# Optimization experiments

Measured on AMD Instinct MI355X. Metric: run time of the kernel, lower is better.

The kernel has to match this reference:

```python
import jax, jax.numpy as jnp
import numpy as np

N, M, D, IN_DIM, RF_DIM, N_REL, L, NQ = 50000, 800000, 64, 768, 768, 500, 2, 2048


def _leaky(x):
    return jnp.where(x >= 0, x, 0.01 * x)  # nn.LeakyReLU default slope


def _ln(x, g, b):
    mu = jnp.mean(x, axis=-1, keepdims=True)
    var = jnp.mean(jnp.square(x - mu), axis=-1, keepdims=True)
    return (x - mu) / jnp.sqrt(var + 1e-5) * g + b


def setup_inputs() -> dict:
    key = jax.random.key(0)
    ks = jax.random.split(key, 24)
    ht = jax.random.randint(ks[0], (M, 2), 0, N)
    # ensure every node receives >= 1 message (avoids 0/0 NaN, as real batches do)
    ht = ht.at[:N, 0].set(jnp.arange(N))
    r_tensor = jax.random.randint(ks[1], (M,), 0, N_REL)
    entity_feat = jax.random.normal(ks[2], (N, IN_DIM), dtype=jnp.float32)
    queries = jnp.zeros((M,), jnp.int32).at[:NQ].set(1)
    s = 0.02
    rel_table = jax.random.normal(ks[3], (N_REL, RF_DIM), dtype=jnp.float32)  # frozen
    inp = {
        "ht": ht, "r_tensor": r_tensor, "entity_feat": entity_feat, "queries": queries,
        "rel_table": rel_table,
        "W_ent": s * jax.random.normal(ks[4], (IN_DIM, D)), "b_ent": jnp.zeros((D,)),
        "g_ent": jnp.ones((D,)), "be_ent": jnp.zeros((D,)),
        "W_edge_in": s * jax.random.normal(ks[5], (RF_DIM, D)), "b_edge_in": jnp.zeros((D,)),
        "g_edge": jnp.ones((D,)), "be_edge": jnp.zeros((D,)),
        "mp_Wf": s * jax.random.normal(ks[6], (L, 2 * D, D)), "mp_bf": jnp.zeros((L, D)),
        "mp_Wb": s * jax.random.normal(ks[7], (L, 2 * D, D)), "mp_bb": jnp.zeros((L, D)),
        "mp_g": jnp.ones((L, D)), "mp_be": jnp.zeros((L, D)),
        "eu_W": s * jax.random.normal(ks[8], (L, 3 * D, D)), "eu_b": jnp.zeros((L, D)),
        "eu_g": jnp.ones((L, D)), "eu_be": jnp.zeros((L, D)),
        "cls_W1": s * jax.random.normal(ks[9], (6 * D, D)), "cls_b1": jnp.zeros((D,)),
        "cls_W2": s * jax.random.normal(ks[10], (D, 1)), "cls_b2": jnp.zeros((1,)),
    }
    return inp


def _forward(ht, r_tensor, queries, rel_table, entity_feat,
             W_ent, b_ent, g_ent, be_ent, W_edge_in, b_edge_in, g_edge, be_edge,
             mp_Wf, mp_bf, mp_Wb, mp_bb, mp_g, mp_be,
             eu_W, eu_b, eu_g, eu_be, cls_W1, cls_b1, cls_W2, cls_b2):
    H0 = _ln(_leaky(entity_feat @ W_ent + b_ent), g_ent, be_ent)      # n x d
    r_embed = rel_table[r_tensor]                                     # m x rf
    E0 = _ln(_leaky(r_embed @ W_edge_in + b_edge_in), g_edge, be_edge)  # m x d
    H, E = H0, E0
    heads, tails = ht[:, 0], ht[:, 1]
    dst = jnp.concatenate([tails, heads])                             # 2m
    ones = jnp.ones((2 * M,), H.dtype)
    cnt = jax.ops.segment_sum(ones, dst, num_segments=N)              # per-node msg count
    for l in range(L):
        # message calculation (fwd uses head reps, back uses tail reps)
        mf = jnp.concatenate([H[heads], E], axis=1) @ mp_Wf[l] + mp_bf[l]
        mb = jnp.concatenate([H[tails], E], axis=1) @ mp_Wb[l] + mp_bb[l]
        msgs = jnp.concatenate([mf, mb], axis=0)                      # 2m x d
        agg = jax.ops.segment_sum(msgs, dst, num_segments=N) / cnt[:, None]
        H = _ln(_leaky(agg) + H, mp_g[l], mp_be[l])
        # edge update
        triple = jnp.concatenate([H[heads], E, H[tails]], axis=1)     # m x 3d
        E = _ln(_leaky(triple @ eu_W[l] + eu_b[l]) + E, eu_g[l], eu_be[l])
    # triple classification on query edges
    qi = jnp.nonzero(queries, size=NQ)[0]
    htq = ht[qi]
    feat = jnp.concatenate([E[qi], E0[qi], H[htq[:, 0]], H0[htq[:, 0]],
                            H[htq[:, 1]], H0[htq[:, 1]]], axis=1)     # NQ x 6d
    out = _leaky(feat @ cls_W1 + cls_b1) @ cls_W2 + cls_b2            # NQ x 1
    return out


def reference(ht, r_tensor, entity_feat, queries, rel_table,
              W_ent, b_ent, g_ent, be_ent, W_edge_in, b_edge_in, g_edge, be_edge,
              mp_Wf, mp_bf, mp_Wb, mp_bb, mp_g, mp_be,
              eu_W, eu_b, eu_g, eu_be, cls_W1, cls_b1, cls_W2, cls_b2):
    return _forward(ht, r_tensor, queries, rel_table, entity_feat,
                    W_ent, b_ent, g_ent, be_ent, W_edge_in, b_edge_in, g_edge, be_edge,
                    mp_Wf, mp_bf, mp_Wb, mp_bb, mp_g, mp_be,
                    eu_W, eu_b, eu_g, eu_be, cls_W1, cls_b1, cls_W2, cls_b2)
```

## Files before the change

kernel.cpp:

```cpp
#include <hip/hip_runtime.h>
#include <hip/hip_bf16.h>
#include <cstdint>

constexpr int IN_DIM = 768;
constexpr int FB_ENT = 0;
constexpr int FB_L0  = 96;
constexpr int FB_L1  = 128;
constexpr int NFRAG  = 160;

typedef __attribute__((ext_vector_type(8))) short bf16x8;
typedef __attribute__((ext_vector_type(4))) float f32x4;

static __device__ __forceinline__ float leaky_(float x){ return x >= 0.0f ? x : 0.01f * x; }

static __device__ __forceinline__ float wsum_(float v){
#pragma unroll
  for (int m = 1; m < 64; m <<= 1) v += __shfl_xor(v, m, 64);
  return v;
}

static __device__ __forceinline__ float wln_(float v, float g, float be){
  float mu  = wsum_(v) * 0.015625f;
  float c   = v - mu;
  float var = wsum_(c * c) * 0.015625f;
  return c * rsqrtf(var + 1e-5f) * g + be;
}

template<int CTRL>
static __device__ __forceinline__ float dpp_radd(float x){
  const int t = __builtin_amdgcn_update_dpp(0, __float_as_int(x), CTRL, 0xf, 0xf, true);
  return x + __int_as_float(t);
}
static __device__ __forceinline__ float rowsum16_(float x){
  x = dpp_radd<0x121>(x);
  x = dpp_radd<0x122>(x);
  x = dpp_radd<0x124>(x);
  x = dpp_radd<0x128>(x);
  return x;
}

static __device__ __forceinline__ unsigned short f2bf(float x){
  return __bfloat16_as_ushort(__float2bfloat16(x));
}
static __device__ __forceinline__ float bf2f(unsigned short u){
  return __bfloat162float(__ushort_as_bfloat16(u));
}
static __device__ __forceinline__ void split4(const float4 a, ushort4& hi, ushort4& lo){
  hi.x = f2bf(a.x); lo.x = f2bf(a.x - bf2f(hi.x));
  hi.y = f2bf(a.y); lo.y = f2bf(a.y - bf2f(hi.y));
  hi.z = f2bf(a.z); lo.z = f2bf(a.z - bf2f(hi.z));
  hi.w = f2bf(a.w); lo.w = f2bf(a.w - bf2f(hi.w));
}

static __device__ __forceinline__ f32x4 mfma3(bf16x8 ah, bf16x8 al, bf16x8 wh, bf16x8 wl, f32x4 acc){
  acc = __builtin_amdgcn_mfma_f32_16x16x32_bf16(ah, wh, acc, 0, 0, 0);
  acc = __builtin_amdgcn_mfma_f32_16x16x32_bf16(al, wh, acc, 0, 0, 0);
  acc = __builtin_amdgcn_mfma_f32_16x16x32_bf16(ah, wl, acc, 0, 0, 0);
  return acc;
}

__global__ __launch_bounds__(256) void k_wprep(
    const float* __restrict__ Went, const float* __restrict__ Wf,
    const float* __restrict__ Wb,
    unsigned short* __restrict__ Fhi, unsigned short* __restrict__ Flo)
{
  const int gt = blockIdx.x * 256 + threadIdx.x;
  if (gt >= NFRAG * 64) return;
  const int fid = gt >> 6, lane = gt & 63;
  int kind, lf;
  if (fid < FB_L0)      { kind = 0; lf = fid; }
  else if (fid < FB_L1) { kind = 1; lf = fid - FB_L0; }
  else                  { kind = 2; lf = fid - FB_L1; }
  const int kt = lf >> 2, nn = lf & 3;
  const int col = nn * 16 + (lane & 15);
  const int r0  = kt * 32 + (lane >> 4) * 8;
  unsigned short* ph = Fhi + ((size_t)fid << 9) + lane * 8;
  unsigned short* pl = Flo + ((size_t)fid << 9) + lane * 8;
#pragma unroll
  for (int j = 0; j < 8; ++j){
    const int gr = r0 + j;
    const float* rp;
    if (kind == 0)      rp = Went + (size_t)gr * 64;
    else if (kind == 1) rp = (gr < 128) ? Wf + (size_t)gr * 64
                                        : Wb + (size_t)(gr - 128) * 64;
    else                rp = (gr < 128) ? Wf + (size_t)(128 + gr) * 64
                                        : Wb + (size_t)gr * 64;
    const float v = rp[col];
    const unsigned short h = f2bf(v);
    ph[j] = h;
    pl[j] = f2bf(v - bf2f(h));
  }
}

__global__ __launch_bounds__(256) void k_encslot(const float* __restrict__ X,
    const unsigned short* __restrict__ Fhi, const unsigned short* __restrict__ Flo,
    const float* __restrict__ b, const float* __restrict__ g_,
    const float* __restrict__ be, float* __restrict__ o0, float* __restrict__ o1,
    int nrows, int encBlocks,
    const int* __restrict__ ht, const int* __restrict__ rt,
    int* __restrict__ posf, int* __restrict__ posb,
    unsigned* __restrict__ si, int M)
{
  __shared__ unsigned short Ahi[64 * 128];
  __shared__ unsigned short Alo[64 * 128];
  const int bid = blockIdx.x;
  const int tid = threadIdx.x;

  if (bid >= encBlocks){
    const int m0 = (bid - encBlocks) * 1024;
    int hv[4], tv[4]; unsigned rsh[4]; bool act[4];
#pragma unroll
    for (int j = 0; j < 4; ++j){
      const int m = m0 + j * 256 + tid;
      act[j] = (m < M);
      const int mm = act[j] ? m : 0;
      hv[j] = ht[2*mm]; tv[j] = ht[2*mm+1];
      rsh[j] = ((unsigned)rt[mm]) << 16;
    }
    int sfi[4], sbi[4];
#pragma unroll
    for (int j = 0; j < 4; ++j) if (act[j]) sfi[j] = atomicAdd(&posf[tv[j]], 1);
#pragma unroll
    for (int j = 0; j < 4; ++j) if (act[j]) sbi[j] = atomicAdd(&posb[hv[j]], 1);
#pragma unroll
    for (int j = 0; j < 4; ++j) if (act[j]) si[sfi[j]] = (unsigned)hv[j] | rsh[j];
#pragma unroll
    for (int j = 0; j < 4; ++j) if (act[j]) si[sbi[j]] = (unsigned)tv[j] | rsh[j];
    return;
  }

  const int tile = bid * 64;
  const int w = tid >> 6, lane = tid & 63, g = lane >> 4, lr = lane & 15;
  const int rowb = w * 16;

  f32x4 acc[4];
#pragma unroll
  for (int n = 0; n < 4; ++n){
    const float bv = b[n * 16 + lr];
    acc[n] = (f32x4){bv, bv, bv, bv};
  }

  for (int ch = 0; ch < 6; ++ch){
    __syncthreads();
#pragma unroll
    for (int i = 0; i < 8; ++i){
      const int idx = tid + 256 * i;
      const int row = idx >> 5, c = idx & 31;
      int gr = tile + row; if (gr >= nrows) gr = nrows - 1;
      const float4 a = *(const float4*)&X[(size_t)gr * IN_DIM + ch * 128 + c * 4];
      ushort4 hi, lo; split4(a, hi, lo);
      const int ad = (row * 256 + c * 8) ^ ((row & 7) << 4);
      *(ushort4*)((char*)Ahi + ad) = hi;
      *(ushort4*)((char*)Alo + ad) = lo;
    }
    __syncthreads();

    bf16x8 Ah[4], Al[4];
#pragma unroll
    for (int kt = 0; kt < 4; ++kt){
      const int row = rowb + lr;
      const int ad = (row * 256 + kt * 64 + g * 16) ^ ((row & 7) << 4);
      Ah[kt] = *(const bf16x8*)((const char*)Ahi + ad);
      Al[kt] = *(const bf16x8*)((const char*)Alo + ad);
    }
    const int fb = ch * 16;
#pragma unroll
    for (int n = 0; n < 4; ++n)
#pragma unroll
      for (int kt = 0; kt < 4; ++kt){
        const size_t fo = (((size_t)(fb + kt * 4 + n)) << 9) + lane * 8;
        acc[n] = mfma3(Ah[kt], Al[kt], *(const bf16x8*)(Fhi + fo), *(const bf16x8*)(Flo + fo), acc[n]);
      }
  }

#pragma unroll
  for (int reg = 0; reg < 4; ++reg){
    const int lrow = rowb + g * 4 + reg;
    float v[4];
#pragma unroll
    for (int n = 0; n < 4; ++n) v[n] = leaky_(acc[n][reg]);
    float s = v[0] + v[1] + v[2] + v[3];
#pragma unroll
    for (int msk = 1; msk < 16; msk <<= 1) s += __shfl_xor(s, msk, 64);
    const float mu = s * 0.015625f;
    float q = 0.f;
#pragma unroll
    for (int n = 0; n < 4; ++n){ v[n] -= mu; q += v[n] * v[n]; }
#pragma unroll
    for (int msk = 1; msk < 16; msk <<= 1) q += __shfl_xor(q, msk, 64);
    const float rs = rsqrtf(q * 0.015625f + 1e-5f);
    const int r = tile + lrow;
    if (r < nrows){
#pragma unroll
      for (int n = 0; n < 4; ++n){
        const int col = n * 16 + lr;
        const float o = v[n] * rs * g_[col] + be[col];
        o0[(size_t)r * 64 + col] = o;
        o1[(size_t)r * 64 + col] = o;
      }
    }
  }
}

__global__ __launch_bounds__(256) void k_hupd2m(float* __restrict__ H,
    const float* __restrict__ Sall,
    const int* __restrict__ cf, const int* __restrict__ cb,
    const unsigned short* __restrict__ Fhi, const unsigned short* __restrict__ Flo, int fb,
    const float* __restrict__ bf, const float* __restrict__ bb,
    const float* __restrict__ g_, const float* __restrict__ be, int N)
{
  __shared__ unsigned short Ahi[64 * 256];
  __shared__ unsigned short Alo[64 * 256];
  const int tile = blockIdx.x * 64, tid = threadIdx.x;
#pragma unroll
  for (int i = 0; i < 16; ++i){
    const int idx = tid + 256 * i;
    const int row = idx >> 6, c = idx & 63;
    int gr = tile + row; if (gr >= N) gr = N - 1;
    const float4 a = *(const float4*)&Sall[(size_t)gr * 256 + c * 4];
    ushort4 hi, lo; split4(a, hi, lo);
    const int ad = (row * 512 + c * 8) ^ ((row & 7) << 4);
    *(ushort4*)((char*)Ahi + ad) = hi;
    *(ushort4*)((char*)Alo + ad) = lo;
  }
  __syncthreads();

  const int w = tid >> 6, lane = tid & 63, g = lane >> 4, lr = lane & 15;
  const int rowb = w * 16;
  bf16x8 Ah[8], Al[8];
#pragma unroll
  for (int kt = 0; kt < 8; ++kt){
    const int row = rowb + lr;
    const int ad = (row * 512 + kt * 64 + g * 16) ^ ((row & 7) << 4);
    Ah[kt] = *(const bf16x8*)((const char*)Ahi + ad);
    Al[kt] = *(const bf16x8*)((const char*)Alo + ad);
  }

  int cfv[4], cbv[4];
#pragma unroll
  for (int reg = 0; reg < 4; ++reg){
    int r = tile + rowb + g * 4 + reg; if (r >= N) r = N - 1;
    cfv[reg] = cf[r]; cbv[reg] = cb[r];
  }
  f32x4 acc[4];
#pragma unroll
  for (int n = 0; n < 4; ++n){
    const float bfc = bf[n * 16 + lr], bbc = bb[n * 16 + lr];
#pragma unroll
    for (int reg = 0; reg < 4; ++reg)
      acc[n][reg] = (float)cfv[reg] * bfc + (float)cbv[reg] * bbc;
  }
#pragma unroll
  for (int n = 0; n < 4; ++n)
#pragma unroll
    for (int kt = 0; kt < 8; ++kt){
      const size_t fo = (((size_t)(fb + kt * 4 + n)) << 9) + lane * 8;
      acc[n] = mfma3(Ah[kt], Al[kt], *(const bf16x8*)(Fhi + fo), *(const bf16x8*)(Flo + fo), acc[n]);
    }

#pragma unroll
  for (int reg = 0; reg < 4; ++reg){
    const int lrow = rowb + g * 4 + reg;
    const int r = tile + lrow;
    const int rr = (r < N) ? r : N - 1;
    const float c = (float)(cfv[reg] + cbv[reg]);
    float v[4];
#pragma unroll
    for (int n = 0; n < 4; ++n)
      v[n] = leaky_(acc[n][reg] / c) + H[(size_t)rr * 64 + n * 16 + lr];
    float s = v[0] + v[1] + v[2] + v[3];
#pragma unroll
    for (int msk = 1; msk < 16; msk <<= 1) s += __shfl_xor(s, msk, 64);
    const float mu = s * 0.015625f;
    float q = 0.f;
#pragma unroll
    for (int n = 0; n < 4; ++n){ v[n] -= mu; q += v[n] * v[n]; }
#pragma unroll
    for (int msk = 1; msk < 16; msk <<= 1) q += __shfl_xor(q, msk, 64);
    const float rs = rsqrtf(q * 0.015625f + 1e-5f);
    if (r < N){
#pragma unroll
      for (int n = 0; n < 4; ++n){
        const int col = n * 16 + lr;
        H[(size_t)r * 64 + col] = v[n] * rs * g_[col] + be[col];
      }
    }
  }
}

__global__ __launch_bounds__(256) void k_enc(const float* __restrict__ X,
    const float* __restrict__ W, const float* __restrict__ b,
    const float* __restrict__ g, const float* __restrict__ be,
    float* __restrict__ o0, float* __restrict__ o1, int nrows)
{
  const int w = threadIdx.x >> 6, d = threadIdx.x & 63;
  const int rbase = blockIdx.x * 16 + w * 4;
  int rows[4];
#pragma unroll
  for (int j = 0; j < 4; ++j){ int r = rbase + j; rows[j] = r < nrows ? r : nrows - 1; }
  float acc[4] = {0.f, 0.f, 0.f, 0.f};
  for (int k4 = 0; k4 < IN_DIM / 4; ++k4){
    const int k = k4 * 4;
    const float w0 = W[(k+0)*64+d], w1 = W[(k+1)*64+d];
    const float w2 = W[(k+2)*64+d], w3 = W[(k+3)*64+d];
#pragma unroll
    for (int j = 0; j < 4; ++j){
      const float4 a = *(const float4*)&X[(size_t)rows[j] * IN_DIM + k];
      acc[j] = fmaf(a.x, w0, fmaf(a.y, w1, fmaf(a.z, w2, fmaf(a.w, w3, acc[j]))));
    }
  }
#pragma unroll
  for (int j = 0; j < 4; ++j){
    const int r = rbase + j;
    if (r < nrows){
      float v = wln_(leaky_(acc[j] + b[d]), g[d], be[d]);
      o0[(size_t)r*64+d] = v;
      if (o1) o1[(size_t)r*64+d] = v;
    }
  }
}

__global__ __launch_bounds__(256) void k_xw2(const float* __restrict__ X,
    const float* __restrict__ W1, const float* __restrict__ W3,
    float* __restrict__ Y, int nrows)
{
  const int w = threadIdx.x >> 6, d = threadIdx.x & 63;
  const int rbase = blockIdx.x * 16 + w * 4;
  int rows[4];
#pragma unroll
  for (int j = 0; j < 4; ++j){ int r = rbase + j; rows[j] = r < nrows ? r : nrows - 1; }
  float a1[4] = {0.f,0.f,0.f,0.f}, a3[4] = {0.f,0.f,0.f,0.f};
  for (int k4 = 0; k4 < 16; ++k4){
    const int k = k4 * 4;
    const float u0 = W1[(k+0)*64+d], u1 = W1[(k+1)*64+d];
    const float u2 = W1[(k+2)*64+d], u3 = W1[(k+3)*64+d];
    const float v0 = W3[(k+0)*64+d], v1 = W3[(k+1)*64+d];
    const float v2 = W3[(k+2)*64+d], v3 = W3[(k+3)*64+d];
#pragma unroll
    for (int j = 0; j < 4; ++j){
      const float4 a = *(const float4*)&X[(size_t)rows[j] * 64 + k];
      a1[j] = fmaf(a.x, u0, fmaf(a.y, u1, fmaf(a.z, u2, fmaf(a.w, u3, a1[j]))));
      a3[j] = fmaf(a.x, v0, fmaf(a.y, v1, fmaf(a.z, v2, fmaf(a.w, v3, a3[j]))));
    }
  }
#pragma unroll
  for (int j = 0; j < 4; ++j){
    const int r = rbase + j;
    if (r < nrows){
      Y[(size_t)r * 128 + d]      = a1[j];
      Y[(size_t)r * 128 + 64 + d] = a3[j];
    }
  }
}

__global__ __launch_bounds__(256) void k_tep(const float* __restrict__ E0t,
    const float* __restrict__ W, const float* __restrict__ bias,
    float2* __restrict__ TEP, int nrows)
{
  const int w = threadIdx.x >> 6, d = threadIdx.x & 63;
  const int rbase = blockIdx.x * 16 + w * 4;
  int rows[4];
#pragma unroll
  for (int j = 0; j < 4; ++j){ int r = rbase + j; rows[j] = r < nrows ? r : nrows - 1; }
  const float b0 = bias[d];
  float acc[4] = {b0, b0, b0, b0};
  for (int k4 = 0; k4 < 16; ++k4){
    const int k = k4 * 4;
    const float w0 = W[(k+0)*64+d], w1 = W[(k+1)*64+d];
    const float w2 = W[(k+2)*64+d], w3 = W[(k+3)*64+d];
#pragma unroll
    for (int j = 0; j < 4; ++j){
      const float4 a = *(const float4*)&E0t[(size_t)rows[j] * 64 + k];
      acc[j] = fmaf(a.x, w0, fmaf(a.y, w1, fmaf(a.z, w2, fmaf(a.w, w3, acc[j]))));
    }
  }
#pragma unroll
  for (int j = 0; j < 4; ++j){
    const int r = rbase + j;
    if (r < nrows) TEP[(size_t)r * 64 + d] = make_float2(acc[j], E0t[(size_t)r * 64 + d]);
  }
}

__global__ __launch_bounds__(256) void k_cnt(const int* __restrict__ ht,
    int* __restrict__ cf, int* __restrict__ cb, int M)
{
  int m = blockIdx.x * 256 + threadIdx.x;
  if (m < M){
    atomicAdd(&cf[ht[2*m+1]], 1);
    atomicAdd(&cb[ht[2*m+0]], 1);
  }
}

__global__ __launch_bounds__(256) void k_scan1(const int* __restrict__ c,
    int* __restrict__ pos, int* __restrict__ bsum, int N)
{
  __shared__ int ws[4];
  const int tid = threadIdx.x, lane = tid & 63, w = tid >> 6;
  const int i = blockIdx.x * 256 + tid;
  const int v = (i < N) ? c[i] : 0;
  int inc = v;
#pragma unroll
  for (int off = 1; off < 64; off <<= 1){
    int t = __shfl_up(inc, off, 64);
    if (lane >= off) inc += t;
  }
  if (lane == 63) ws[w] = inc;
  __syncthreads();
  int wbase = 0;
  for (int j = 0; j < w; ++j) wbase += ws[j];
  if (i < N) pos[i] = wbase + inc - v;
  if (tid == 255) bsum[blockIdx.x] = wbase + inc;
}

__global__ __launch_bounds__(256) void k_scan3(int* __restrict__ pos,
    const int* __restrict__ bsum, int N, int offset)
{
  const int i = blockIdx.x * 256 + threadIdx.x;
  if (i < N) pos[i] += bsum[blockIdx.x] + offset;
}

__global__ __launch_bounds__(256) void k_qscan(int* __restrict__ bcnt, int nb)
{
  __shared__ int ws[4];
  const int tid = threadIdx.x, lane = tid & 63, w = tid >> 6;
  const int chunk = (nb + 255) / 256;
  int s = 0;
  for (int i = 0; i < chunk; ++i){ int idx = tid * chunk + i; if (idx < nb) s += bcnt[idx]; }
  int v = s;
#pragma unroll
  for (int off = 1; off < 64; off <<= 1){ int t = __shfl_up(v, off, 64); if (lane >= off) v += t; }
  if (lane == 63) ws[w] = v;
  __syncthreads();
  int wbase = 0;
  for (int i = 0; i < w; ++i) wbase += ws[i];
  int run = wbase + v - s;
  for (int i = 0; i < chunk; ++i){
    int idx = tid * chunk + i;
    if (idx < nb){ int t = bcnt[idx]; bcnt[idx] = run; run += t; }
  }
}

static __device__ __forceinline__ void qmerge_(f32x4& a){
#pragma unroll
  for (int c = 0; c < 4; ++c){
    float x = a[c];
    x += __shfl_xor(x, 16, 64);
    x += __shfl_xor(x, 32, 64);
    a[c] = x;
  }
}

__global__ __launch_bounds__(256) void k_sum(const float* __restrict__ H,
    const float* __restrict__ E, const unsigned* __restrict__ si,
    const int* __restrict__ posf_end, const int* __restrict__ posb_end,
    const int* __restrict__ cf, const int* __restrict__ cb,
    float* __restrict__ Sall, int N)
{
  const int w = threadIdx.x >> 6, lane = threadIdx.x & 63;
  const int n = blockIdx.x * 4 + w;
  if (n >= N) return;
  const int q = lane >> 4, l16 = lane & 15;
  f32x4 sf = {0,0,0,0}, ef = {0,0,0,0}, sb = {0,0,0,0}, eb = {0,0,0,0};
  {
    const int end = posf_end[n], start = end - cf[n];
#pragma unroll 2
    for (int i0 = start; i0 < end; i0 += 4){
      int i = i0 + q;
      const bool act = (i < end); if (!act) i = end - 1;
      const unsigned sv = si[i];
      const int src = (int)(sv & 0xffffu), r = (int)(sv >> 16);
      const float4 h4 = *(const float4*)&H[(size_t)src * 64 + l16 * 4];
      const float4 e4 = *(const float4*)&E[(size_t)r * 64 + l16 * 4];
      const float p = act ? 1.f : 0.f;
      sf[0] = fmaf(p, h4.x, sf[0]); sf[1] = fmaf(p, h4.y, sf[1]);
      sf[2] = fmaf(p, h4.z, sf[2]); sf[3] = fmaf(p, h4.w, sf[3]);
      ef[0] = fmaf(p, e4.x, ef[0]); ef[1] = fmaf(p, e4.y, ef[1]);
      ef[2] = fmaf(p, e4.z, ef[2]); ef[3] = fmaf(p, e4.w, ef[3]);
    }
  }
  {
    const int end = posb_end[n], start = end - cb[n];
#pragma unroll 2
    for (int i0 = start; i0 < end; i0 += 4){
      int i = i0 + q;
      const bool act = (i < end); if (!act) i = end - 1;
      const unsigned sv = si[i];
      const int src = (int)(sv & 0xffffu), r = (int)(sv >> 16);
      const float4 h4 = *(const float4*)&H[(size_t)src * 64 + l16 * 4];
      const float4 e4 = *(const float4*)&E[(size_t)r * 64 + l16 * 4];
      const float p = act ? 1.f : 0.f;
      sb[0] = fmaf(p, h4.x, sb[0]); sb[1] = fmaf(p, h4.y, sb[1]);
      sb[2] = fmaf(p, h4.z, sb[2]); sb[3] = fmaf(p, h4.w, sb[3]);
      eb[0] = fmaf(p, e4.x, eb[0]); eb[1] = fmaf(p, e4.y, eb[1]);
      eb[2] = fmaf(p, e4.z, eb[2]); eb[3] = fmaf(p, e4.w, eb[3]);
    }
  }
  qmerge_(sf); qmerge_(ef); qmerge_(sb); qmerge_(eb);
  if (q == 0){
    float* S = Sall + (size_t)n * 256;
    *(f32x4*)&S[      l16 * 4] = sf;
    *(f32x4*)&S[ 64 + l16 * 4] = ef;
    *(f32x4*)&S[128 + l16 * 4] = sb;
    *(f32x4*)&S[192 + l16 * 4] = eb;
  }
}

__global__ __launch_bounds__(256) void k_sum2(const float* __restrict__ H,
    const float* __restrict__ HWp, const float2* __restrict__ TEP,
    const unsigned* __restrict__ si,
    const int* __restrict__ posf_end, const int* __restrict__ posb_end,
    const int* __restrict__ cf, const int* __restrict__ cb,
    const float* __restrict__ g0, const float* __restrict__ be0,
    float* __restrict__ Sall, int N)
{
  const int w = threadIdx.x >> 6, lane = threadIdx.x & 63;
  const int n = blockIdx.x * 4 + w;
  if (n >= N) return;
  const int q = lane >> 4, l16 = lane & 15;
  const float4 gg4  = *(const float4*)&g0 [l16 * 4];
  const float4 bb4  = *(const float4*)&be0[l16 * 4];
  const float4 h1n4 = *(const float4*)&HWp[(size_t)n * 128 +      l16 * 4];
  const float4 h3n4 = *(const float4*)&HWp[(size_t)n * 128 + 64 + l16 * 4];
  f32x4 sf = {0,0,0,0}, ef = {0,0,0,0}, sb = {0,0,0,0}, eb = {0,0,0,0};

#define SUM2_LOOP(POS_END, CNT, OTH_OFF, N0, N1, N2, N3, SACC, EACC)            \
  {                                                                             \
    const int end = POS_END[n], start = end - CNT[n];                           \
    _Pragma("unroll 2")                                                         \
    for (int i0 = start; i0 < end; i0 += 4){                                    \
      int i = i0 + q;                                                           \
      const bool act = (i < end); if (!act) i = end - 1;                        \
      const unsigned sv = si[i];                                                \
      const int src = (int)(sv & 0xffffu), rr_ = (int)(sv >> 16);               \
      const float4 h4 = *(const float4*)&H[(size_t)src * 64 + l16 * 4];         \
      const float4 o4 = *(const float4*)&HWp[(size_t)src * 128 + OTH_OFF + l16 * 4]; \
      const float* tp = (const float*)&TEP[(size_t)rr_ * 64 + l16 * 4];         \
      const float4 t0 = *(const float4*)&tp[0];                                 \
      const float4 t1 = *(const float4*)&tp[4];                                 \
      float v[4];                                                               \
      v[0] = leaky_(o4.x + N0 + t0.x) + t0.y;                                   \
      v[1] = leaky_(o4.y + N1 + t0.z) + t0.w;                                   \
      v[2] = leaky_(o4.z + N2 + t1.x) + t1.y;                                   \
      v[3] = leaky_(o4.w + N3 + t1.z) + t1.w;                                   \
      float s  = (v[0] + v[1]) + (v[2] + v[3]);                                 \
      float qq = fmaf(v[0], v[0], v[1] * v[1]) + fmaf(v[2], v[2], v[3] * v[3]); \
      s  = rowsum16_(s);                                                        \
      qq = rowsum16_(qq);                                                       \
      const float mu  = s * 0.015625f;                                          \
      const float var = fmaxf(qq * 0.015625f - mu * mu, 0.f);                   \
      const float rsg = rsqrtf(var + 1e-5f);                                    \
      const float p = act ? 1.f : 0.f;                                          \
      SACC[0] = fmaf(p, h4.x, SACC[0]); SACC[1] = fmaf(p, h4.y, SACC[1]);       \
      SACC[2] = fmaf(p, h4.z, SACC[2]); SACC[3] = fmaf(p, h4.w, SACC[3]);       \
      _Pragma("unroll")                                                         \
      for (int c = 0; c < 4; ++c){                                              \
        const float e1 = (v[c] - mu) * rsg * ((const float*)&gg4)[c]            \
                       + ((const float*)&bb4)[c];                               \
        EACC[c] = fmaf(p, e1, EACC[c]);                                         \
      }                                                                         \
    }                                                                           \
  }

  SUM2_LOOP(posf_end, cf, 0,  h3n4.x, h3n4.y, h3n4.z, h3n4.w, sf, ef)
  SUM2_LOOP(posb_end, cb, 64, h1n4.x, h1n4.y, h1n4.z, h1n4.w, sb, eb)
#undef SUM2_LOOP

  qmerge_(sf); qmerge_(ef); qmerge_(sb); qmerge_(eb);
  if (q == 0){
    float* S = Sall + (size_t)n * 256;
    *(f32x4*)&S[      l16 * 4] = sf;
    *(f32x4*)&S[ 64 + l16 * 4] = ef;
    *(f32x4*)&S[128 + l16 * 4] = sb;
    *(f32x4*)&S[192 + l16 * 4] = eb;
  }
}

__global__ __launch_bounds__(256) void k_eu2q(const float* __restrict__ HWp,
    const float2* __restrict__ TEP, const int* __restrict__ ht,
    const int* __restrict__ rt, const int* __restrict__ qi,
    const float* __restrict__ g, const float* __restrict__ be,
    float* __restrict__ e1q, int NQ)
{
  const int w = threadIdx.x >> 6, lane = threadIdx.x & 63;
  const int row = blockIdx.x * 4 + w;
  if (row >= NQ) return;
  const int m = qi[row];
  const int h = ht[2*m], t = ht[2*m+1], r = rt[m];
  const float2 te = TEP[(size_t)r * 64 + lane];
  float v = HWp[(size_t)h*128+lane] + HWp[(size_t)t*128+64+lane] + te.x;
  v = leaky_(v) + te.y;
  e1q[(size_t)row*64+lane] = wln_(v, g[lane], be[lane]);
}

__global__ __launch_bounds__(256) void k_qcount(const int* __restrict__ q,
                                                int* __restrict__ bcnt, int M)
{
  const int j = blockIdx.x * 256 + threadIdx.x;
  const int have = (j < M) && (q[j] != 0);
  unsigned long long bal = __ballot(have);
  if ((threadIdx.x & 63) == 0) atomicAdd(&bcnt[blockIdx.x], (int)__popcll(bal));
}

__global__ __launch_bounds__(256) void k_qemit(const int* __restrict__ q,
    const int* __restrict__ bcnt, int* __restrict__ qi, int M, int NQ)
{
  __shared__ int wb[4];
  const int j = blockIdx.x * 256 + threadIdx.x;
  const int lane = threadIdx.x & 63, w = threadIdx.x >> 6;
  const int have = (j < M) && (q[j] != 0);
  unsigned long long bal = __ballot(have);
  if (lane == 0) wb[w] = (int)__popcll(bal);
  __syncthreads();
  int base = bcnt[blockIdx.x];
  for (int i = 0; i < w; ++i) base += wb[i];
  const int rank = base + (int)__popcll(bal & ((1ull << lane) - 1ull));
  if (have && rank < NQ) qi[rank] = j;
}

__global__ __launch_bounds__(256) void k_feat(
    const float* __restrict__ H, const float* __restrict__ H0,
    const float* __restrict__ e1q, const float* __restrict__ E0t,
    const int* __restrict__ rt, const int* __restrict__ ht, const int* __restrict__ qi,
    const float* __restrict__ W, const float* __restrict__ b,
    const float* __restrict__ g, const float* __restrict__ be,
    float* __restrict__ feat, int NQ)
{
  const int w = threadIdx.x >> 6, d = threadIdx.x & 63;
  const int row = blockIdx.x * 4 + w;
  if (row >= NQ) return;
  const int m = qi[row];
  const int h = ht[2*m], t = ht[2*m+1], r = rt[m];
  const float* seg0 = H   + (size_t)h * 64;
  const float* seg1 = e1q + (size_t)row * 64;
  const float* seg2 = H   + (size_t)t * 64;
  float acc = b[d];
  for (int k4 = 0; k4 < 48; ++k4){
    const int k = k4 * 4;
    const float* A = (k4 < 16) ? seg0 : (k4 < 32) ? seg1 - 64 : seg2 - 128;
    const float4 a = *(const float4*)&A[k];
    acc = fmaf(a.x, W[(k+0)*64+d], fmaf(a.y, W[(k+1)*64+d],
          fmaf(a.z, W[(k+2)*64+d], fmaf(a.w, W[(k+3)*64+d], acc))));
  }
  const float ep = seg1[d];
  const float e2 = wln_(leaky_(acc) + ep, g[d], be[d]);
  float* F = feat + (size_t)row * 384;
  F[      d] = e2;
  F[ 64 + d] = E0t[(size_t)r*64+d];
  F[128 + d] = H [(size_t)h*64+d];
  F[192 + d] = H0[(size_t)h*64+d];
  F[256 + d] = H [(size_t)t*64+d];
  F[320 + d] = H0[(size_t)t*64+d];
}

__global__ __launch_bounds__(256) void k_cls(const float* __restrict__ feat,
    const float* __restrict__ W1, const float* __restrict__ b1,
    const float* __restrict__ W2, const float* __restrict__ b2,
    float* __restrict__ out, int NQ)
{
  const int w = threadIdx.x >> 6, d = threadIdx.x & 63;
  const int row = blockIdx.x * 4 + w;
  if (row >= NQ) return;
  const float* F = feat + (size_t)row * 384;
  float acc = b1[d];
  for (int k4 = 0; k4 < 96; ++k4){
    const int k = k4 * 4;
    const float4 a = *(const float4*)&F[k];
    acc = fmaf(a.x, W1[(k+0)*64+d], fmaf(a.y, W1[(k+1)*64+d],
          fmaf(a.z, W1[(k+2)*64+d], fmaf(a.w, W1[(k+3)*64+d], acc))));
  }
  float hs = leaky_(acc) * W2[d];
  hs = wsum_(hs);
  if (d == 0) out[row] = hs + b2[0];
}

extern "C" void kernel_launch(void* const* d_in, const int* in_sizes, int n_in,
                              void* d_out, int out_size, void* d_ws, size_t ws_size,
                              hipStream_t stream)
{
  const int*   ht    = (const int*)  d_in[0];
  const int*   rt    = (const int*)  d_in[1];
  const float* ef    = (const float*)d_in[2];
  const int*   q     = (const int*)  d_in[3];
  const float* rtab  = (const float*)d_in[4];
  const float* W_ent = (const float*)d_in[5];
  const float* b_ent = (const float*)d_in[6];
  const float* g_ent = (const float*)d_in[7];
  const float* be_ent= (const float*)d_in[8];
  const float* W_ein = (const float*)d_in[9];
  const float* b_ein = (const float*)d_in[10];
  const float* g_e   = (const float*)d_in[11];
  const float* be_e  = (const float*)d_in[12];
  const float* mp_Wf = (const float*)d_in[13];
  const float* mp_bf = (const float*)d_in[14];
  const float* mp_Wb = (const float*)d_in[15];
  const float* mp_bb = (const float*)d_in[16];
  const float* mp_g  = (const float*)d_in[17];
  const float* mp_be = (const float*)d_in[18];
  const float* eu_W  = (const float*)d_in[19];
  const float* eu_b  = (const float*)d_in[20];
  const float* eu_g  = (const float*)d_in[21];
  const float* eu_be = (const float*)d_in[22];
  const float* clsW1 = (const float*)d_in[23];
  const float* clsb1 = (const float*)d_in[24];
  const float* clsW2 = (const float*)d_in[25];
  const float* clsb2 = (const float*)d_in[26];

  const int M    = in_sizes[1];
  const int N    = in_sizes[2] / IN_DIM;
  const int NREL = in_sizes[4] / IN_DIM;
  const int NQ   = out_size;
  const int nb   = (M + 255) / 256;
  const int nbn  = (N + 255) / 256;

  unsigned short* Fhi = (unsigned short*)d_ws;
  unsigned short* Flo = Fhi + (size_t)NFRAG * 512;
  float* H0    = (float*)(Flo + (size_t)NFRAG * 512);
  float* H     = H0    + (size_t)N * 64;
  float* HWp   = H     + (size_t)N * 64;
  float* Sall  = HWp   + (size_t)N * 128;
  float* E0t   = Sall  + (size_t)N * 256;
  float2* TEP  = (float2*)(E0t + (size_t)NREL * 64);
  float* e1q   = (float*)(TEP + (size_t)NREL * 64);
  float* feat  = e1q   + (size_t)NQ * 64;
  int*   cf    = (int*)(feat + (size_t)NQ * 384);
  int*   cb    = cf + N;
  int*   posf  = cb + N;
  int*   posb  = posf + N;
  unsigned* si = (unsigned*)(posb + N);
  int*   qi    = (int*)(si + 2 * (size_t)M);
  int*   bcnt  = qi + NQ;
  int*   bsumf = bcnt + nb;
  int*   bsumb = bsumf + nbn;

  hipMemsetAsync(cf,   0, (size_t)N  * 4, stream);
  hipMemsetAsync(cb,   0, (size_t)N  * 4, stream);
  hipMemsetAsync(qi,   0, (size_t)NQ * 4, stream);
  hipMemsetAsync(bcnt, 0, (size_t)nb * 4, stream);

  k_wprep<<<(NFRAG * 64 + 255) / 256, 256, 0, stream>>>(W_ent, mp_Wf, mp_Wb, Fhi, Flo);
  k_cnt<<<(M + 255) / 256, 256, 0, stream>>>(ht, cf, cb, M);
  k_scan1<<<nbn, 256, 0, stream>>>(cf, posf, bsumf, N);
  k_qscan<<<1, 256, 0, stream>>>(bsumf, nbn);
  k_scan3<<<nbn, 256, 0, stream>>>(posf, bsumf, N, 0);
  k_scan1<<<nbn, 256, 0, stream>>>(cb, posb, bsumb, N);
  k_qscan<<<1, 256, 0, stream>>>(bsumb, nbn);
  k_scan3<<<nbn, 256, 0, stream>>>(posb, bsumb, N, M);

  const int encBlocks = (N + 63) / 64;
  const int slotBlocks = (M + 1023) / 1024;
  k_encslot<<<encBlocks + slotBlocks, 256, 0, stream>>>(ef, Fhi, Flo,
      b_ent, g_ent, be_ent, H0, H, N, encBlocks, ht, rt, posf, posb, si, M);

  k_enc<<<(NREL + 15) / 16, 256, 0, stream>>>(rtab, W_ein, b_ein, g_e, be_e, E0t, nullptr, NREL);
  k_tep<<<(NREL + 15) / 16, 256, 0, stream>>>(E0t, eu_W + 64 * 64, eu_b, TEP, NREL);

  const int sgrid = (N + 3) / 4;
  k_sum<<<sgrid, 256, 0, stream>>>(H, E0t, si, posf, posb, cf, cb, Sall, N);
  k_hupd2m<<<(N + 63) / 64, 256, 0, stream>>>(H, Sall, cf, cb, Fhi, Flo, FB_L0,
      mp_bf, mp_bb, mp_g, mp_be, N);
  k_xw2<<<(N + 15) / 16, 256, 0, stream>>>(H, eu_W, eu_W + 128 * 64, HWp, N);

  k_sum2<<<sgrid, 256, 0, stream>>>(H, HWp, TEP, si, posf, posb, cf, cb,
      eu_g, eu_be, Sall, N);

  k_qcount<<<nb, 256, 0, stream>>>(q, bcnt, M);
  k_qscan<<<1, 256, 0, stream>>>(bcnt, nb);
  k_qemit<<<nb, 256, 0, stream>>>(q, bcnt, qi, M, NQ);
  k_eu2q<<<(NQ + 3) / 4, 256, 0, stream>>>(HWp, TEP, ht, rt, qi,
      eu_g, eu_be, e1q, NQ);

  k_hupd2m<<<(N + 63) / 64, 256, 0, stream>>>(H, Sall, cf, cb, Fhi, Flo, FB_L1,
      mp_bf + 64, mp_bb + 64, mp_g + 64, mp_be + 64, N);

  k_feat<<<(NQ + 3) / 4, 256, 0, stream>>>(H, H0, e1q, E0t, rt, ht, qi,
      eu_W + 192 * 64, eu_b + 64, eu_g + 64, eu_be + 64, feat, NQ);
  k_cls<<<(NQ + 3) / 4, 256, 0, stream>>>(feat, clsW1, clsb1, clsW2, clsb2,
      (float*)d_out, NQ);
}
```

Baseline: 652.4 us.

## Fuse layer-0 node update with edge-update projections using MFMA

Replaces the separate layer-0 node update and the scalar FP32 H@W1/H@W3 projection kernel with one fused kernel. After computing and layer-normalizing the new H tile, the kernel writes it back to shared memory as a bf16 hi/lo split and runs the two edge-update projections with split-bf16 MFMA. The weight prep kernel now also builds fragments for these two projections. This saves a kernel launch and a full re-read of H, and moves the projection from scalar FMAs to matrix cores. The cost is a larger LDS footprint and extra register pressure in the fused kernel, and the three-term bf16 split gives slightly different precision from the FP32 loop.

```diff
diff --git a/kernel.cpp b/kernel.cpp
--- a/kernel.cpp
+++ b/kernel.cpp
@@ -6,7 +6,9 @@
 constexpr int FB_ENT = 0;
 constexpr int FB_L0  = 96;
 constexpr int FB_L1  = 128;
-constexpr int NFRAG  = 160;
+constexpr int FB_EU1 = 160;
+constexpr int FB_EU3 = 168;
+constexpr int NFRAG  = 176;
 
 typedef __attribute__((ext_vector_type(8))) short bf16x8;
 typedef __attribute__((ext_vector_type(4))) float f32x4;
@@ -61,16 +63,18 @@
 
 __global__ __launch_bounds__(256) void k_wprep(
     const float* __restrict__ Went, const float* __restrict__ Wf,
-    const float* __restrict__ Wb,
+    const float* __restrict__ Wb, const float* __restrict__ euW,
     unsigned short* __restrict__ Fhi, unsigned short* __restrict__ Flo)
 {
   const int gt = blockIdx.x * 256 + threadIdx.x;
   if (gt >= NFRAG * 64) return;
   const int fid = gt >> 6, lane = gt & 63;
   int kind, lf;
-  if (fid < FB_L0)      { kind = 0; lf = fid; }
-  else if (fid < FB_L1) { kind = 1; lf = fid - FB_L0; }
-  else                  { kind = 2; lf = fid - FB_L1; }
+  if (fid < FB_L0)       { kind = 0; lf = fid; }
+  else if (fid < FB_L1)  { kind = 1; lf = fid - FB_L0; }
+  else if (fid < FB_EU1) { kind = 2; lf = fid - FB_L1; }
+  else if (fid < FB_EU3) { kind = 3; lf = fid - FB_EU1; }
+  else                   { kind = 4; lf = fid - FB_EU3; }
   const int kt = lf >> 2, nn = lf & 3;
   const int col = nn * 16 + (lane & 15);
   const int r0  = kt * 32 + (lane >> 4) * 8;
@@ -83,8 +87,10 @@
     if (kind == 0)      rp = Went + (size_t)gr * 64;
     else if (kind == 1) rp = (gr < 128) ? Wf + (size_t)gr * 64
                                         : Wb + (size_t)(gr - 128) * 64;
-    else                rp = (gr < 128) ? Wf + (size_t)(128 + gr) * 64
+    else if (kind == 2) rp = (gr < 128) ? Wf + (size_t)(128 + gr) * 64
                                         : Wb + (size_t)gr * 64;
+    else if (kind == 3) rp = euW + (size_t)gr * 64;
+    else                rp = euW + (size_t)(128 + gr) * 64;
     const float v = rp[col];
     const unsigned short h = f2bf(v);
     ph[j] = h;
@@ -288,6 +294,132 @@
   }
 }
 
+__global__ __launch_bounds__(256) void k_hupd2mx(float* __restrict__ H,
+    const float* __restrict__ Sall,
+    const int* __restrict__ cf, const int* __restrict__ cb,
+    const unsigned short* __restrict__ Fhi, const unsigned short* __restrict__ Flo,
+    const float* __restrict__ bf, const float* __restrict__ bb,
+    const float* __restrict__ g_, const float* __restrict__ be,
+    float* __restrict__ HWp, int N)
+{
+  __shared__ unsigned short Ahi[64 * 256];
+  __shared__ unsigned short Alo[64 * 256];
+  const int tile = blockIdx.x * 64, tid = threadIdx.x;
+#pragma unroll
+  for (int i = 0; i < 16; ++i){
+    const int idx = tid + 256 * i;
+    const int row = idx >> 6, c = idx & 63;
+    int gr = tile + row; if (gr >= N) gr = N - 1;
+    const float4 a = *(const float4*)&Sall[(size_t)gr * 256 + c * 4];
+    ushort4 hi, lo; split4(a, hi, lo);
+    const int ad = (row * 512 + c * 8) ^ ((row & 7) << 4);
+    *(ushort4*)((char*)Ahi + ad) = hi;
+    *(ushort4*)((char*)Alo + ad) = lo;
+  }
+  __syncthreads();
+
+  const int w = tid >> 6, lane = tid & 63, g = lane >> 4, lr = lane & 15;
+  const int rowb = w * 16;
+  bf16x8 Ah[8], Al[8];
+#pragma unroll
+  for (int kt = 0; kt < 8; ++kt){
+    const int row = rowb + lr;
+    const int ad = (row * 512 + kt * 64 + g * 16) ^ ((row & 7) << 4);
+    Ah[kt] = *(const bf16x8*)((const char*)Ahi + ad);
+    Al[kt] = *(const bf16x8*)((const char*)Alo + ad);
+  }
+
+  int cfv[4], cbv[4];
+#pragma unroll
+  for (int reg = 0; reg < 4; ++reg){
+    int r = tile + rowb + g * 4 + reg; if (r >= N) r = N - 1;
+    cfv[reg] = cf[r]; cbv[reg] = cb[r];
+  }
+  f32x4 acc[4];
+#pragma unroll
+  for (int n = 0; n < 4; ++n){
+    const float bfc = bf[n * 16 + lr], bbc = bb[n * 16 + lr];
+#pragma unroll
+    for (int reg = 0; reg < 4; ++reg)
+      acc[n][reg] = (float)cfv[reg] * bfc + (float)cbv[reg] * bbc;
+  }
+#pragma unroll
+  for (int n = 0; n < 4; ++n)
+#pragma unroll
+    for (int kt = 0; kt < 8; ++kt){
+      const size_t fo = (((size_t)(FB_L0 + kt * 4 + n)) << 9) + lane * 8;
+      acc[n] = mfma3(Ah[kt], Al[kt], *(const bf16x8*)(Fhi + fo), *(const bf16x8*)(Flo + fo), acc[n]);
+    }
+
+  __syncthreads();
+
+#pragma unroll
+  for (int reg = 0; reg < 4; ++reg){
+    const int lrow = rowb + g * 4 + reg;
+    const int r = tile + lrow;
+    const int rr = (r < N) ? r : N - 1;
+    const float c = (float)(cfv[reg] + cbv[reg]);
+    float v[4];
+#pragma unroll
+    for (int n = 0; n < 4; ++n)
+      v[n] = leaky_(acc[n][reg] / c) + H[(size_t)rr * 64 + n * 16 + lr];
+    float s = v[0] + v[1] + v[2] + v[3];
+#pragma unroll
+    for (int msk = 1; msk < 16; msk <<= 1) s += __shfl_xor(s, msk, 64);
+    const float mu = s * 0.015625f;
+    float q = 0.f;
+#pragma unroll
+    for (int n = 0; n < 4; ++n){ v[n] -= mu; q += v[n] * v[n]; }
+#pragma unroll
+    for (int msk = 1; msk < 16; msk <<= 1) q += __shfl_xor(q, msk, 64);
+    const float rs = rsqrtf(q * 0.015625f + 1e-5f);
+#pragma unroll
+    for (int n = 0; n < 4; ++n){
+      const int col = n * 16 + lr;
+      const float o = v[n] * rs * g_[col] + be[col];
+      if (r < N) H[(size_t)r * 64 + col] = o;
+      const int ad2 = (lrow * 128 + col * 2) ^ ((lrow & 7) << 4);
+      const unsigned short hh = f2bf(o);
+      *(unsigned short*)((char*)Ahi + ad2) = hh;
+      *(unsigned short*)((char*)Alo + ad2) = f2bf(o - bf2f(hh));
+    }
+  }
+  __syncthreads();
+
+  bf16x8 Bh[2], Bl[2];
+#pragma unroll
+  for (int kt = 0; kt < 2; ++kt){
+    const int row = rowb + lr;
+    const int ad = (row * 128 + kt * 64 + g * 16) ^ ((row & 7) << 4);
+    Bh[kt] = *(const bf16x8*)((const char*)Ahi + ad);
+    Bl[kt] = *(const bf16x8*)((const char*)Alo + ad);
+  }
+  f32x4 a1[4], a3[4];
+#pragma unroll
+  for (int n = 0; n < 4; ++n){ a1[n] = (f32x4){0,0,0,0}; a3[n] = (f32x4){0,0,0,0}; }
+#pragma unroll
+  for (int n = 0; n < 4; ++n)
+#pragma unroll
+    for (int kt = 0; kt < 2; ++kt){
+      const size_t f1 = (((size_t)(FB_EU1 + kt * 4 + n)) << 9) + lane * 8;
+      const size_t f3 = (((size_t)(FB_EU3 + kt * 4 + n)) << 9) + lane * 8;
+      a1[n] = mfma3(Bh[kt], Bl[kt], *(const bf16x8*)(Fhi + f1), *(const bf16x8*)(Flo + f1), a1[n]);
+      a3[n] = mfma3(Bh[kt], Bl[kt], *(const bf16x8*)(Fhi + f3), *(const bf16x8*)(Flo + f3), a3[n]);
+    }
+#pragma unroll
+  for (int reg = 0; reg < 4; ++reg){
+    const int r = tile + rowb + g * 4 + reg;
+    if (r < N){
+#pragma unroll
+      for (int n = 0; n < 4; ++n){
+        const int col = n * 16 + lr;
+        HWp[(size_t)r * 128 + col]      = a1[n][reg];
+        HWp[(size_t)r * 128 + 64 + col] = a3[n][reg];
+      }
+    }
+  }
+}
+
 __global__ __launch_bounds__(256) void k_enc(const float* __restrict__ X,
     const float* __restrict__ W, const float* __restrict__ b,
     const float* __restrict__ g, const float* __restrict__ be,
@@ -316,39 +448,6 @@
       float v = wln_(leaky_(acc[j] + b[d]), g[d], be[d]);
       o0[(size_t)r*64+d] = v;
       if (o1) o1[(size_t)r*64+d] = v;
-    }
-  }
-}
-
-__global__ __launch_bounds__(256) void k_xw2(const float* __restrict__ X,
-    const float* __restrict__ W1, const float* __restrict__ W3,
-    float* __restrict__ Y, int nrows)
-{
-  const int w = threadIdx.x >> 6, d = threadIdx.x & 63;
-  const int rbase = blockIdx.x * 16 + w * 4;
-  int rows[4];
-#pragma unroll
-  for (int j = 0; j < 4; ++j){ int r = rbase + j; rows[j] = r < nrows ? r : nrows - 1; }
-  float a1[4] = {0.f,0.f,0.f,0.f}, a3[4] = {0.f,0.f,0.f,0.f};
-  for (int k4 = 0; k4 < 16; ++k4){
-    const int k = k4 * 4;
-    const float u0 = W1[(k+0)*64+d], u1 = W1[(k+1)*64+d];
-    const float u2 = W1[(k+2)*64+d], u3 = W1[(k+3)*64+d];
-    const float v0 = W3[(k+0)*64+d], v1 = W3[(k+1)*64+d];
-    const float v2 = W3[(k+2)*64+d], v3 = W3[(k+3)*64+d];
-#pragma unroll
-    for (int j = 0; j < 4; ++j){
-      const float4 a = *(const float4*)&X[(size_t)rows[j] * 64 + k];
-      a1[j] = fmaf(a.x, u0, fmaf(a.y, u1, fmaf(a.z, u2, fmaf(a.w, u3, a1[j]))));
-      a3[j] = fmaf(a.x, v0, fmaf(a.y, v1, fmaf(a.z, v2, fmaf(a.w, v3, a3[j]))));
-    }
-  }
-#pragma unroll
-  for (int j = 0; j < 4; ++j){
-    const int r = rbase + j;
-    if (r < nrows){
-      Y[(size_t)r * 128 + d]      = a1[j];
-      Y[(size_t)r * 128 + 64 + d] = a3[j];
     }
   }
 }
@@ -737,7 +836,7 @@
   hipMemsetAsync(qi,   0, (size_t)NQ * 4, stream);
   hipMemsetAsync(bcnt, 0, (size_t)nb * 4, stream);
 
-  k_wprep<<<(NFRAG * 64 + 255) / 256, 256, 0, stream>>>(W_ent, mp_Wf, mp_Wb, Fhi, Flo);
+  k_wprep<<<(NFRAG * 64 + 255) / 256, 256, 0, stream>>>(W_ent, mp_Wf, mp_Wb, eu_W, Fhi, Flo);
   k_cnt<<<(M + 255) / 256, 256, 0, stream>>>(ht, cf, cb, M);
   k_scan1<<<nbn, 256, 0, stream>>>(cf, posf, bsumf, N);
   k_qscan<<<1, 256, 0, stream>>>(bsumf, nbn);
@@ -756,9 +855,8 @@
 
   const int sgrid = (N + 3) / 4;
   k_sum<<<sgrid, 256, 0, stream>>>(H, E0t, si, posf, posb, cf, cb, Sall, N);
-  k_hupd2m<<<(N + 63) / 64, 256, 0, stream>>>(H, Sall, cf, cb, Fhi, Flo, FB_L0,
-      mp_bf, mp_bb, mp_g, mp_be, N);
-  k_xw2<<<(N + 15) / 16, 256, 0, stream>>>(H, eu_W, eu_W + 128 * 64, HWp, N);
+  k_hupd2mx<<<(N + 63) / 64, 256, 0, stream>>>(H, Sall, cf, cb, Fhi, Flo,
+      mp_bf, mp_bb, mp_g, mp_be, HWp, N);
 
   k_sum2<<<sgrid, 256, 0, stream>>>(H, HWp, TEP, si, posf, posb, cf, cb,
       eu_g, eu_be, Sall, N);
```

Measured after the change: 610.2 us. 6.5% less time.
